# Kernel tuning notes

Hardware: AMD Instinct MI355X
Metric: run time of the kernel (lower is better)

## Reference

```python
import jax, jax.numpy as jnp
import numpy as np

N_POINTS = 1_000_000
NUM_SEGMENTS = 100_000
D_IN = 64
FEA_COMPRE = 16  # linear: 64 -> 2*fea_compre = 32


def setup_inputs() -> dict:
    key = jax.random.key(0)
    k1, k2, k3, k4, k5 = jax.random.split(key, 5)
    shuffled_ind = jax.random.permutation(k1, N_POINTS)  # shuffle of point rows
    pt_gfeatures = jax.random.normal(k2, (N_POINTS, D_IN), dtype=jnp.float32)
    pt_localfeatures2 = jax.random.normal(k3, (N_POINTS, D_IN), dtype=jnp.float32)
    pt_inv = jnp.sort(jax.random.randint(k4, (N_POINTS,), 0, NUM_SEGMENTS))
    W = jax.random.normal(k5, (D_IN, 2 * FEA_COMPRE), dtype=jnp.float32) * (1.0 / np.sqrt(D_IN))
    b = jnp.zeros((2 * FEA_COMPRE,), dtype=jnp.float32)
    return {
        "shuffled_ind": shuffled_ind,
        "pt_gfeatures": pt_gfeatures,
        "pt_localfeatures2": pt_localfeatures2,
        "pt_inv": pt_inv,
        "W": W,
        "b": b,
    }


def reference(shuffled_ind, pt_gfeatures, pt_localfeatures2, pt_inv, W, b):
    # gather + add fused expression: [N, 64]
    x = pt_gfeatures[shuffled_ind, :] + pt_localfeatures2
    # scatter_max over segments: [M, 64]
    pooled = jax.ops.segment_max(x, pt_inv, num_segments=NUM_SEGMENTS)
    # empty segments come back as -inf; torch_scatter leaves them at fill value -> use 0
    pooled = jnp.where(jnp.isfinite(pooled), pooled, jnp.zeros((), pooled.dtype))
    # fea_compre*2 = 32 is in (0, 64), so the compression branch runs
    return jax.nn.relu(pooled @ W + b)  # [M, 32]
```

## Files before the change

### kernel.cpp

```cpp
#include <hip/hip_runtime.h>
#include <hip/hip_bf16.h>
#include <math.h>


#define D_IN 64
#define K_OUT 32
#define RPW 128
#define WPB 4
#define ENC_NEG_INF 0x007FFFFFu

__device__ __forceinline__ unsigned enc_f32(float f) {
    unsigned u = __float_as_uint(f);
    return (u & 0x80000000u) ? ~u : (u | 0x80000000u);
}
__device__ __forceinline__ float dec_f32(unsigned u) {
    unsigned b = (u & 0x80000000u) ? (u ^ 0x80000000u) : ~u;
    return __uint_as_float(b);
}

__global__ __launch_bounds__(256) void init_pooled_kernel(uint4* __restrict__ p, int n4)
{
    const uint4 v = make_uint4(ENC_NEG_INF, ENC_NEG_INF, ENC_NEG_INF, ENC_NEG_INF);
    for (int i = blockIdx.x * blockDim.x + threadIdx.x; i < n4; i += gridDim.x * blockDim.x)
        p[i] = v;
}

__global__ __launch_bounds__(64 * WPB) void scan_max_kernel(
    const int*   __restrict__ shuffled_ind,
    const float* __restrict__ g,
    const float* __restrict__ l,
    const int*   __restrict__ pt_inv,
    unsigned*    __restrict__ pooled,
    int n)
{
    __shared__ int ind_lds[WPB][RPW];
    __shared__ int seg_lds[WPB][RPW];

    const int tid  = threadIdx.x;
    const int wid  = tid >> 6;
    const int lane = tid & 63;
    const int base = (blockIdx.x * WPB + wid) * RPW;
    const int rows = min(RPW, n - base);

    #pragma unroll
    for (int j0 = 0; j0 < RPW; j0 += 64) {
        const int r = j0 + lane;
        if (r < rows) {
            ind_lds[wid][r] = shuffled_ind[base + r];
            seg_lds[wid][r] = pt_inv[base + r];
        }
    }
    __syncthreads();
    if (rows <= 0) return;

    int   curSeg   = seg_lds[wid][0];
    int   segFirst = 0;
    float m        = -INFINITY;

    for (int i0 = 0; i0 < rows; i0 += 8) {
        float x[8];
        #pragma unroll
        for (int k = 0; k < 8; ++k) {
            const int i  = min(i0 + k, rows - 1);
            const int ind = ind_lds[wid][i];
            x[k] = g[(size_t)ind * D_IN + lane] + l[(size_t)(base + i) * D_IN + lane];
        }
        #pragma unroll
        for (int k = 0; k < 8; ++k) {
            const int i = i0 + k;
            if (i < rows) {
                const int seg = seg_lds[wid][i];
                if (seg != curSeg) {
                    unsigned* p = pooled + (size_t)curSeg * D_IN + lane;
                    const unsigned e = enc_f32(m);
                    if (segFirst == 0) atomicMax(p, e); else *p = e;
                    curSeg = seg; segFirst = i; m = x[k];
                } else {
                    m = fmaxf(m, x[k]);
                }
            }
        }
    }
    atomicMax(pooled + (size_t)curSeg * D_IN + lane, enc_f32(m));
}

__global__ __launch_bounds__(256) void gemm_kernel(
    const unsigned* __restrict__ pooled,
    const float*    __restrict__ W,
    const float*    __restrict__ b,
    float*          __restrict__ out,
    int M)
{
    __shared__ float Ws[D_IN * K_OUT];
    __shared__ float bs[K_OUT];
    __shared__ float pool[WPB][D_IN];

    const int tid = threadIdx.x;
    for (int i = tid; i < D_IN * K_OUT; i += 64 * WPB) Ws[i] = W[i];
    if (tid < K_OUT) bs[tid] = b[tid];

    const int wid  = tid >> 6;
    const int lane = tid & 63;
    const int s    = blockIdx.x * WPB + wid;
    const bool active = (s < M);

    if (active) {
        const unsigned u = pooled[(size_t)s * D_IN + lane];
        pool[wid][lane] = (u == ENC_NEG_INF) ? 0.0f : dec_f32(u);
    }
    __syncthreads();

    if (active && lane < K_OUT) {
        float acc = bs[lane];
        #pragma unroll
        for (int c = 0; c < D_IN; ++c)
            acc = fmaf(pool[wid][c], Ws[c * K_OUT + lane], acc);
        out[(size_t)s * K_OUT + lane] = fmaxf(acc, 0.0f);
    }
}

__global__ __launch_bounds__(256) void seg_starts_kernel(
    const int* __restrict__ pt_inv, int n, int* __restrict__ starts, int M)
{
    int s = blockIdx.x * blockDim.x + threadIdx.x;
    if (s > M) return;
    int lo = 0, hi = n;
    while (lo < hi) { int mid = (lo + hi) >> 1; if (pt_inv[mid] < s) lo = mid + 1; else hi = mid; }
    starts[s] = lo;
}

__global__ __launch_bounds__(256) void pool_gemm_kernel(
    const int* __restrict__ shuffled_ind, const float* __restrict__ g,
    const float* __restrict__ l, const int* __restrict__ starts,
    const float* __restrict__ W, const float* __restrict__ b,
    float* __restrict__ out, int M)
{
    __shared__ float Ws[D_IN * K_OUT];
    __shared__ float bs[K_OUT];
    __shared__ float pool[WPB][D_IN];
    const int tid = threadIdx.x;
    for (int i = tid; i < D_IN * K_OUT; i += 64 * WPB) Ws[i] = W[i];
    if (tid < K_OUT) bs[tid] = b[tid];
    const int wid = tid >> 6, lane = tid & 63;
    const int s = blockIdx.x * WPB + wid;
    const bool active = (s < M);
    float m = -INFINITY;
    if (active) {
        const int p0 = starts[s], p1 = starts[s + 1];
        for (int p = p0; p < p1; ++p) {
            const int ind = shuffled_ind[p];
            m = fmaxf(m, g[(size_t)ind * D_IN + lane] + l[(size_t)p * D_IN + lane]);
        }
        if (p1 <= p0) m = 0.0f;
    }
    if (active) pool[wid][lane] = m;
    __syncthreads();
    if (active && lane < K_OUT) {
        float acc = bs[lane];
        #pragma unroll
        for (int c = 0; c < D_IN; ++c) acc = fmaf(pool[wid][c], Ws[c * K_OUT + lane], acc);
        out[(size_t)s * K_OUT + lane] = fmaxf(acc, 0.0f);
    }
}

extern "C" void kernel_launch(void* const* d_in, const int* in_sizes, int n_in,
                              void* d_out, int out_size, void* d_ws, size_t ws_size,
                              hipStream_t stream)
{
    const int*   shuffled_ind = (const int*)  d_in[0];
    const float* g            = (const float*)d_in[1];
    const float* l            = (const float*)d_in[2];
    const int*   pt_inv       = (const int*)  d_in[3];
    const float* W            = (const float*)d_in[4];
    const float* b            = (const float*)d_in[5];
    float*       out          = (float*)d_out;

    const int N = in_sizes[0];
    const int M = out_size / K_OUT;

    const size_t pooled_bytes = (size_t)M * D_IN * sizeof(unsigned);

    if (ws_size >= pooled_bytes) {
        unsigned* pooled = (unsigned*)d_ws;
        {
            const int n4 = (int)(pooled_bytes / 16);
            init_pooled_kernel<<<512, 256, 0, stream>>>((uint4*)pooled, n4);
        }
        {
            const int rows_per_block = WPB * RPW;
            const int blocks = (N + rows_per_block - 1) / rows_per_block;
            scan_max_kernel<<<blocks, 64 * WPB, 0, stream>>>(
                shuffled_ind, g, l, pt_inv, pooled, N);
        }
        {
            const int blocks = (M + WPB - 1) / WPB;
            gemm_kernel<<<blocks, 64 * WPB, 0, stream>>>(pooled, W, b, out, M);
        }
    } else {
        int* starts = (int*)d_ws;
        {
            const int blocks = (M + 1 + 255) / 256;
            seg_starts_kernel<<<blocks, 256, 0, stream>>>(pt_inv, N, starts, M);
        }
        {
            const int blocks = (M + WPB - 1) / WPB;
            pool_gemm_kernel<<<blocks, 64 * WPB, 0, stream>>>(
                shuffled_ind, g, l, starts, W, b, out, M);
        }
    }
}
```

Baseline: 179.9 us.

## Vectorize scan-max with float4 row-group loads and two-segment GEMM waves

Restructures the scan-max kernel so each wave handles four rows per step: each 16-lane quarter loads one row as float4 from both gathered and local features. A three-deep register prefetch pipeline hides gather latency, and a fast path skips per-row segment checks when all four rows share a segment. Flushes reduce across quarters with xor shuffles before writing. The GEMM kernel now processes two segments per wave so all 64 lanes do useful work. The change aims to cut instruction count and raise memory-level parallelism, at the cost of extra shuffles on segment boundaries and more complex control flow.

After: 160.3 us. -10.9%, faster.

```diff
diff --git a/kernel.cpp b/kernel.cpp
--- a/kernel.cpp
+++ b/kernel.cpp
@@ -39,6 +39,8 @@
     const int tid  = threadIdx.x;
     const int wid  = tid >> 6;
     const int lane = tid & 63;
+    const int rp   = lane >> 4;
+    const int cg   = lane & 15;
     const int base = (blockIdx.x * WPB + wid) * RPW;
     const int rows = min(RPW, n - base);
 
@@ -53,35 +55,74 @@
     __syncthreads();
     if (rows <= 0) return;
 
-    int   curSeg   = seg_lds[wid][0];
-    int   segFirst = 0;
-    float m        = -INFINITY;
-
-    for (int i0 = 0; i0 < rows; i0 += 8) {
-        float x[8];
-        #pragma unroll
-        for (int k = 0; k < 8; ++k) {
-            const int i  = min(i0 + k, rows - 1);
-            const int ind = ind_lds[wid][i];
-            x[k] = g[(size_t)ind * D_IN + lane] + l[(size_t)(base + i) * D_IN + lane];
-        }
-        #pragma unroll
-        for (int k = 0; k < 8; ++k) {
-            const int i = i0 + k;
-            if (i < rows) {
-                const int seg = seg_lds[wid][i];
-                if (seg != curSeg) {
-                    unsigned* p = pooled + (size_t)curSeg * D_IN + lane;
-                    const unsigned e = enc_f32(m);
-                    if (segFirst == 0) atomicMax(p, e); else *p = e;
-                    curSeg = seg; segFirst = i; m = x[k];
-                } else {
-                    m = fmaxf(m, x[k]);
-                }
+    const int rl      = rows - 1;
+    const int ngroups = (rows + 3) >> 2;
+
+    int    curSeg   = seg_lds[wid][0];
+    bool   firstRun = true;
+    float4 m4 = make_float4(-INFINITY, -INFINITY, -INFINITY, -INFINITY);
+
+    auto load_group = [&](int grp) -> float4 {
+        const int irow = min(grp * 4 + rp, rl);
+        const int ind  = ind_lds[wid][irow];
+        const float4 gv = *reinterpret_cast<const float4*>(g + (size_t)ind * D_IN + cg * 4);
+        const float4 lv = *reinterpret_cast<const float4*>(l + (size_t)(base + irow) * D_IN + cg * 4);
+        return make_float4(gv.x + lv.x, gv.y + lv.y, gv.z + lv.z, gv.w + lv.w);
+    };
+    auto acc4 = [&](const float4& x) {
+        m4.x = fmaxf(m4.x, x.x); m4.y = fmaxf(m4.y, x.y);
+        m4.z = fmaxf(m4.z, x.z); m4.w = fmaxf(m4.w, x.w);
+    };
+    auto do_flush = [&](int seg, bool useAtomic) {
+        float4 t = m4;
+        t.x = fmaxf(t.x, __shfl_xor(t.x, 16)); t.y = fmaxf(t.y, __shfl_xor(t.y, 16));
+        t.z = fmaxf(t.z, __shfl_xor(t.z, 16)); t.w = fmaxf(t.w, __shfl_xor(t.w, 16));
+        t.x = fmaxf(t.x, __shfl_xor(t.x, 32)); t.y = fmaxf(t.y, __shfl_xor(t.y, 32));
+        t.z = fmaxf(t.z, __shfl_xor(t.z, 32)); t.w = fmaxf(t.w, __shfl_xor(t.w, 32));
+        if (rp == 0) {
+            unsigned* p = pooled + (size_t)seg * D_IN + cg * 4;
+            const unsigned ex = enc_f32(t.x), ey = enc_f32(t.y),
+                           ez = enc_f32(t.z), ew = enc_f32(t.w);
+            if (useAtomic) {
+                atomicMax(p + 0, ex); atomicMax(p + 1, ey);
+                atomicMax(p + 2, ez); atomicMax(p + 3, ew);
+            } else {
+                *reinterpret_cast<uint4*>(p) = make_uint4(ex, ey, ez, ew);
             }
         }
-    }
-    atomicMax(pooled + (size_t)curSeg * D_IN + lane, enc_f32(m));
+    };
+
+    float4 xA = load_group(0);
+    float4 xB = load_group(1);
+    float4 xC = load_group(2);
+
+    for (int grp = 0; grp < ngroups; ++grp) {
+        float4 xD = load_group(grp + 3);
+
+        const int i0 = grp * 4;
+        const int s3 = seg_lds[wid][min(i0 + 3, rl)];
+        if (s3 == curSeg) {
+            acc4(xA);
+        } else {
+            const int s0 = seg_lds[wid][min(i0 + 0, rl)];
+            const int s1 = seg_lds[wid][min(i0 + 1, rl)];
+            const int s2 = seg_lds[wid][min(i0 + 2, rl)];
+            if (s0 != curSeg) { do_flush(curSeg, firstRun); firstRun = false; curSeg = s0;
+                                m4 = make_float4(-INFINITY,-INFINITY,-INFINITY,-INFINITY); }
+            if (rp == 0) acc4(xA);
+            if (s1 != curSeg) { do_flush(curSeg, firstRun); firstRun = false; curSeg = s1;
+                                m4 = make_float4(-INFINITY,-INFINITY,-INFINITY,-INFINITY); }
+            if (rp == 1) acc4(xA);
+            if (s2 != curSeg) { do_flush(curSeg, firstRun); firstRun = false; curSeg = s2;
+                                m4 = make_float4(-INFINITY,-INFINITY,-INFINITY,-INFINITY); }
+            if (rp == 2) acc4(xA);
+            if (s3 != curSeg) { do_flush(curSeg, firstRun); firstRun = false; curSeg = s3;
+                                m4 = make_float4(-INFINITY,-INFINITY,-INFINITY,-INFINITY); }
+            if (rp == 3) acc4(xA);
+        }
+        xA = xB; xB = xC; xC = xD;
+    }
+    do_flush(curSeg, true);
 }
 
 __global__ __launch_bounds__(256) void gemm_kernel(
@@ -93,29 +134,36 @@
 {
     __shared__ float Ws[D_IN * K_OUT];
     __shared__ float bs[K_OUT];
-    __shared__ float pool[WPB][D_IN];
+    __shared__ float pool[WPB][2 * D_IN];
 
     const int tid = threadIdx.x;
-    for (int i = tid; i < D_IN * K_OUT; i += 64 * WPB) Ws[i] = W[i];
+    for (int i = tid; i < D_IN * K_OUT; i += 256) Ws[i] = W[i];
     if (tid < K_OUT) bs[tid] = b[tid];
 
     const int wid  = tid >> 6;
     const int lane = tid & 63;
-    const int s    = blockIdx.x * WPB + wid;
-    const bool active = (s < M);
-
-    if (active) {
-        const unsigned u = pooled[(size_t)s * D_IN + lane];
-        pool[wid][lane] = (u == ENC_NEG_INF) ? 0.0f : dec_f32(u);
+    const int s0   = (blockIdx.x * WPB + wid) * 2;
+
+    if (s0 < M) {
+        const int nvals = min(2, M - s0) * D_IN;
+        uint2 u = make_uint2(ENC_NEG_INF, ENC_NEG_INF);
+        if (lane * 2 < nvals)
+            u = *reinterpret_cast<const uint2*>(pooled + (size_t)s0 * D_IN + lane * 2);
+        pool[wid][lane * 2 + 0] = (u.x == ENC_NEG_INF) ? 0.0f : dec_f32(u.x);
+        pool[wid][lane * 2 + 1] = (u.y == ENC_NEG_INF) ? 0.0f : dec_f32(u.y);
     }
     __syncthreads();
 
-    if (active && lane < K_OUT) {
-        float acc = bs[lane];
+    const int h = lane >> 5;
+    const int k = lane & 31;
+    const int s = s0 + h;
+    if (s0 < M && s < M) {
+        float acc = bs[k];
+        const float* pr = &pool[wid][h * D_IN];
         #pragma unroll
         for (int c = 0; c < D_IN; ++c)
-            acc = fmaf(pool[wid][c], Ws[c * K_OUT + lane], acc);
-        out[(size_t)s * K_OUT + lane] = fmaxf(acc, 0.0f);
+            acc = fmaf(pr[c], Ws[c * K_OUT + k], acc);
+        out[(size_t)s * K_OUT + k] = fmaxf(acc, 0.0f);
     }
 }
 
@@ -139,7 +187,7 @@
     __shared__ float bs[K_OUT];
     __shared__ float pool[WPB][D_IN];
     const int tid = threadIdx.x;
-    for (int i = tid; i < D_IN * K_OUT; i += 64 * WPB) Ws[i] = W[i];
+    for (int i = tid; i < D_IN * K_OUT; i += 256) Ws[i] = W[i];
     if (tid < K_OUT) bs[tid] = b[tid];
     const int wid = tid >> 6, lane = tid & 63;
     const int s = blockIdx.x * WPB + wid;
@@ -193,7 +241,7 @@
                 shuffled_ind, g, l, pt_inv, pooled, N);
         }
         {
-            const int blocks = (M + WPB - 1) / WPB;
+            const int blocks = (M + 2 * WPB - 1) / (2 * WPB);
             gemm_kernel<<<blocks, 64 * WPB, 0, stream>>>(pooled, W, b, out, M);
         }
     } else {
```

## Stream gathered rows into LDS via async global_load_lds double-buffered pipeline

Applied to the files above, without the earlier changes.

Replaces the scan-max kernel with one where each wave handles 64 rows and pulls gathered g rows and l rows straight into LDS using global_load_lds 16-byte transfers. A two-stage double buffer with explicit vmcnt waits overlaps loads with the max scan, and finished segment runs are buffered in LDS and written out in batches. The GEMM kernel now handles two segments per wave with vectorized uint2 loads. The new path requires N to be a multiple of 64 and depends on hand-placed waitcnt ordering, which is fragile.

New measurement: 153.6 us. 14.6% less time.

```diff
diff --git a/kernel.cpp b/kernel.cpp
--- a/kernel.cpp
+++ b/kernel.cpp
@@ -5,9 +5,13 @@
 
 #define D_IN 64
 #define K_OUT 32
-#define RPW 128
 #define WPB 4
+#define RW 64
+#define QMAX 16
 #define ENC_NEG_INF 0x007FFFFFu
+
+typedef __attribute__((address_space(3))) uint32_t lds_u32_t;
+typedef __attribute__((address_space(1))) uint32_t glb_u32_t;
 
 __device__ __forceinline__ unsigned enc_f32(float f) {
     unsigned u = __float_as_uint(f);
@@ -18,6 +22,10 @@
     return __uint_as_float(b);
 }
 
+__device__ __forceinline__ void dma16(const float* gsrc, float* ldst) {
+    __builtin_amdgcn_global_load_lds((const glb_u32_t*)gsrc, (lds_u32_t*)ldst, 16, 0, 0);
+}
+
 __global__ __launch_bounds__(256) void init_pooled_kernel(uint4* __restrict__ p, int n4)
 {
     const uint4 v = make_uint4(ENC_NEG_INF, ENC_NEG_INF, ENC_NEG_INF, ENC_NEG_INF);
@@ -25,97 +33,147 @@
         p[i] = v;
 }
 
-__global__ __launch_bounds__(64 * WPB) void scan_max_kernel(
-    const int*   __restrict__ shuffled_ind,
+__device__ __noinline__ void drain_runs(
+    float (*obv)[64], int* obs, unsigned* __restrict__ pooled,
+    int lane, int nq, int runBase, int isFinal)
+{
+    for (int q = 0; q < nq; ++q) {
+        const float v  = obv[q][lane];
+        const int   sg = obs[q];
+        const int   runId = runBase + q;
+        const bool  at = (runId == 0) || (isFinal && (q == nq - 1));
+        unsigned* p = pooled + (size_t)sg * D_IN + lane;
+        const unsigned e = enc_f32(v);
+        if (at) atomicMax(p, e);
+        else    *p = e;
+    }
+}
+
+__global__ __launch_bounds__(256) void scan_dma_kernel(
+    const int*   __restrict__ ind_arr,
     const float* __restrict__ g,
     const float* __restrict__ l,
-    const int*   __restrict__ pt_inv,
+    const int*   __restrict__ seg_arr,
     unsigned*    __restrict__ pooled,
     int n)
 {
-    __shared__ int ind_lds[WPB][RPW];
-    __shared__ int seg_lds[WPB][RPW];
+    __shared__ __align__(16) float pipe[WPB][2][2][512];
+    __shared__ __align__(16) float obv[WPB][QMAX][64];
+    __shared__ int obs[WPB][QMAX];
 
     const int tid  = threadIdx.x;
     const int wid  = tid >> 6;
     const int lane = tid & 63;
-    const int base = (blockIdx.x * WPB + wid) * RPW;
-    const int rows = min(RPW, n - base);
-
+    const int gw   = blockIdx.x * WPB + wid;
+    const int wbase = gw * RW;
+    if (wbase >= n) return;
+
+    int idx[16];
     #pragma unroll
-    for (int j0 = 0; j0 < RPW; j0 += 64) {
-        const int r = j0 + lane;
-        if (r < rows) {
-            ind_lds[wid][r] = shuffled_ind[base + r];
-            seg_lds[wid][r] = pt_inv[base + r];
-        }
-    }
-    __syncthreads();
-    if (rows <= 0) return;
-
-    int   curSeg   = seg_lds[wid][0];
-    int   segFirst = 0;
-    float m        = -INFINITY;
-
-    for (int i0 = 0; i0 < rows; i0 += 8) {
-        float x[8];
-        #pragma unroll
-        for (int k = 0; k < 8; ++k) {
-            const int i  = min(i0 + k, rows - 1);
-            const int ind = ind_lds[wid][i];
-            x[k] = g[(size_t)ind * D_IN + lane] + l[(size_t)(base + i) * D_IN + lane];
-        }
-        #pragma unroll
-        for (int k = 0; k < 8; ++k) {
-            const int i = i0 + k;
-            if (i < rows) {
-                const int seg = seg_lds[wid][i];
-                if (seg != curSeg) {
-                    unsigned* p = pooled + (size_t)curSeg * D_IN + lane;
-                    const unsigned e = enc_f32(m);
-                    if (segFirst == 0) atomicMax(p, e); else *p = e;
-                    curSeg = seg; segFirst = i; m = x[k];
-                } else {
-                    m = fmaxf(m, x[k]);
-                }
-            }
-        }
-    }
-    atomicMax(pooled + (size_t)curSeg * D_IN + lane, enc_f32(m));
+    for (int k = 0; k < 16; ++k)
+        idx[k] = ind_arr[wbase + 4 * k + (lane >> 4)];
+    const int segv = seg_arr[wbase + lane];
+
+    float m   = -INFINITY;
+    int   cur = __shfl(segv, 0);
+    int   nq = 0, runBase = 0;
+
+    const int cg4 = (lane & 15) << 2;
+    const int l4  = lane << 2;
+
+#define WAITV4 asm volatile("s_waitcnt vmcnt(4)" ::: "memory")
+#define WAITV0 asm volatile("s_waitcnt vmcnt(0)" ::: "memory")
+#define LGKM0  asm volatile("s_waitcnt lgkmcnt(0)" ::: "memory")
+
+#define ISSUE(s) do {                                                          \
+    float* bg_ = &pipe[wid][(s) & 1][0][0];                                    \
+    float* bl_ = &pipe[wid][(s) & 1][1][0];                                    \
+    dma16(g + (size_t)idx[2*(s)    ] * D_IN + cg4, bg_);                       \
+    dma16(g + (size_t)idx[2*(s) + 1] * D_IN + cg4, bg_ + 256);                 \
+    dma16(l + ((size_t)wbase + 8*(s)    ) * D_IN + l4, bl_);                   \
+    dma16(l + ((size_t)wbase + 8*(s) + 4) * D_IN + l4, bl_ + 256);             \
+} while (0)
+
+    auto FLUSH = [&]() {
+        if (nq == QMAX) {
+            LGKM0;
+            drain_runs(&obv[wid][0], &obs[wid][0], pooled, lane, nq, runBase, 0);
+            runBase += nq; nq = 0;
+            WAITV0;
+        }
+        obv[wid][nq][lane] = m;
+        if (lane == 0) obs[wid][nq] = cur;
+        ++nq;
+    };
+
+#define ROWSTEP(s, j) do {                                                     \
+    const float x_ = pipe[wid][(s)&1][0][(j)*64 + lane]                        \
+                   + pipe[wid][(s)&1][1][(j)*64 + lane];                       \
+    const int sr_ = __shfl(segv, (s)*8 + (j));                                 \
+    if (sr_ != cur) { FLUSH(); cur = sr_; m = x_; }                            \
+    else            { m = fmaxf(m, x_); }                                      \
+} while (0)
+
+#define CONS(s) do { ROWSTEP(s,0); ROWSTEP(s,1); ROWSTEP(s,2); ROWSTEP(s,3);   \
+                     ROWSTEP(s,4); ROWSTEP(s,5); ROWSTEP(s,6); ROWSTEP(s,7); } while (0)
+
+    ISSUE(0); ISSUE(1);
+    WAITV4;  CONS(0); LGKM0; ISSUE(2);
+    WAITV4;  CONS(1); LGKM0; ISSUE(3);
+    WAITV4;  CONS(2); LGKM0; ISSUE(4);
+    WAITV4;  CONS(3); LGKM0; ISSUE(5);
+    WAITV4;  CONS(4); LGKM0; ISSUE(6);
+    WAITV4;  CONS(5); LGKM0; ISSUE(7);
+    WAITV4;  CONS(6);
+    WAITV0;  CONS(7);
+    FLUSH();
+    LGKM0;
+    drain_runs(&obv[wid][0], &obs[wid][0], pooled, lane, nq, runBase, 1);
+
+#undef ISSUE
+#undef ROWSTEP
+#undef CONS
+#undef WAITV4
+#undef WAITV0
+#undef LGKM0
 }
 
 __global__ __launch_bounds__(256) void gemm_kernel(
-    const unsigned* __restrict__ pooled,
-    const float*    __restrict__ W,
-    const float*    __restrict__ b,
-    float*          __restrict__ out,
-    int M)
+    const unsigned* __restrict__ pooled, const float* __restrict__ W,
+    const float* __restrict__ b, float* __restrict__ out, int M)
 {
     __shared__ float Ws[D_IN * K_OUT];
     __shared__ float bs[K_OUT];
-    __shared__ float pool[WPB][D_IN];
+    __shared__ float pool[WPB][2 * D_IN];
 
     const int tid = threadIdx.x;
-    for (int i = tid; i < D_IN * K_OUT; i += 64 * WPB) Ws[i] = W[i];
+    for (int i = tid; i < D_IN * K_OUT; i += 256) Ws[i] = W[i];
     if (tid < K_OUT) bs[tid] = b[tid];
 
     const int wid  = tid >> 6;
     const int lane = tid & 63;
-    const int s    = blockIdx.x * WPB + wid;
-    const bool active = (s < M);
-
-    if (active) {
-        const unsigned u = pooled[(size_t)s * D_IN + lane];
-        pool[wid][lane] = (u == ENC_NEG_INF) ? 0.0f : dec_f32(u);
+    const int s0   = (blockIdx.x * WPB + wid) * 2;
+
+    if (s0 < M) {
+        const int nvals = min(2, M - s0) * D_IN;
+        uint2 u = make_uint2(ENC_NEG_INF, ENC_NEG_INF);
+        if (lane * 2 < nvals)
+            u = *reinterpret_cast<const uint2*>(pooled + (size_t)s0 * D_IN + lane * 2);
+        pool[wid][lane * 2 + 0] = (u.x == ENC_NEG_INF) ? 0.0f : dec_f32(u.x);
+        pool[wid][lane * 2 + 1] = (u.y == ENC_NEG_INF) ? 0.0f : dec_f32(u.y);
     }
     __syncthreads();
 
-    if (active && lane < K_OUT) {
-        float acc = bs[lane];
+    const int h = lane >> 5;
+    const int k = lane & 31;
+    const int s = s0 + h;
+    if (s0 < M && s < M) {
+        float acc = bs[k];
+        const float* pr = &pool[wid][h * D_IN];
         #pragma unroll
         for (int c = 0; c < D_IN; ++c)
-            acc = fmaf(pool[wid][c], Ws[c * K_OUT + lane], acc);
-        out[(size_t)s * K_OUT + lane] = fmaxf(acc, 0.0f);
+            acc = fmaf(pr[c], Ws[c * K_OUT + k], acc);
+        out[(size_t)s * K_OUT + k] = fmaxf(acc, 0.0f);
     }
 }
 
@@ -139,7 +197,7 @@
     __shared__ float bs[K_OUT];
     __shared__ float pool[WPB][D_IN];
     const int tid = threadIdx.x;
-    for (int i = tid; i < D_IN * K_OUT; i += 64 * WPB) Ws[i] = W[i];
+    for (int i = tid; i < D_IN * K_OUT; i += 256) Ws[i] = W[i];
     if (tid < K_OUT) bs[tid] = b[tid];
     const int wid = tid >> 6, lane = tid & 63;
     const int s = blockIdx.x * WPB + wid;
@@ -180,20 +238,20 @@
 
     const size_t pooled_bytes = (size_t)M * D_IN * sizeof(unsigned);
 
-    if (ws_size >= pooled_bytes) {
+    if (ws_size >= pooled_bytes && (N % RW) == 0 && N >= RW) {
         unsigned* pooled = (unsigned*)d_ws;
         {
             const int n4 = (int)(pooled_bytes / 16);
             init_pooled_kernel<<<512, 256, 0, stream>>>((uint4*)pooled, n4);
         }
         {
-            const int rows_per_block = WPB * RPW;
-            const int blocks = (N + rows_per_block - 1) / rows_per_block;
-            scan_max_kernel<<<blocks, 64 * WPB, 0, stream>>>(
+            const int waves  = N / RW;
+            const int blocks = (waves + WPB - 1) / WPB;
+            scan_dma_kernel<<<blocks, 64 * WPB, 0, stream>>>(
                 shuffled_ind, g, l, pt_inv, pooled, N);
         }
         {
-            const int blocks = (M + WPB - 1) / WPB;
+            const int blocks = (M + 2 * WPB - 1) / (2 * WPB);
             gemm_kernel<<<blocks, 64 * WPB, 0, stream>>>(pooled, W, b, out, M);
         }
     } else {
```
